# Optimization experiments

Measured on AMD Instinct MI355X. Metric: run time of the kernel, lower is better.

The kernel has to match this reference:

```python
import jax, jax.numpy as jnp
import numpy as np

B = 64          # batch
C = 80          # num_classes
IN_CH = 300     # word-embedding channel
J = 8192        # JOINT_EMB_SIZE (linear_intermediate)
S = 8           # pooling_stride
OUT = J // S    # out_in_tmp = 1024


def setup_inputs() -> dict:
    key = jax.random.key(0)
    ks = jax.random.split(key, 8)
    w = lambda k, sh: jax.random.normal(k, sh, jnp.float32) * 0.02
    return {
        "feature": jax.random.normal(ks[0], (B, 2048, 14, 14), jnp.float32),
        "inp": jax.random.normal(ks[1], (1, C, IN_CH), jnp.float32),
        "A": jax.random.uniform(ks[2], (C, C), jnp.float32),  # positive co-occurrence adjacency
        "W_gc1": w(ks[3], (IN_CH, 1024)),
        "W_gc2": w(ks[4], (1024, 2048)),
        "W_img": w(ks[5], (J, 2048)),
        "b_img": jnp.zeros((J,), jnp.float32),
        "W_cls": w(ks[6], (J, 2048)),
        "b_cls": jnp.zeros((J,), jnp.float32),
        "W_ml": w(ks[7], (C, C * OUT)),
        "b_ml": jnp.zeros((C,), jnp.float32),
    }


def reference(feature, inp, A, W_gc1, W_gc2, W_img, b_img, W_cls, b_cls, W_ml, b_ml):
    # backbone output -> MaxPool2d(14,14) over a 14x14 map == global spatial max
    feat = feature.max(axis=(2, 3))                       # [B, 2048]

    # gen_adj(A).detach(): D = diag(rowsum(A)^-0.5); adj = D @ A.T @ D
    dinv = jnp.sum(A, axis=1) ** -0.5                     # [C]
    adj = jax.lax.stop_gradient(A.T * dinv[:, None] * dinv[None, :])  # [C, C]

    # two GCN layers on label embeddings
    x = adj @ (inp[0] @ W_gc1)                            # [C, 1024]
    x = jax.nn.leaky_relu(x, 0.2)
    x = adj @ (x @ W_gc2)                                 # [C, 2048]

    # MFB bilinear fusion (vectorized form of the nested batch/class loops;
    # dropout is identity in eval mode)
    img = feat @ W_img.T + b_img                          # [B, J]
    cls = x @ W_cls.T + b_cls                             # [C, J]
    # sum-pool over the stride axis of the elementwise product:
    # iq[b,c,o] = sum_s img[b,o*S+s] * cls[c,o*S+s]
    pooled = jnp.einsum('bos,cos->bco',
                        img.reshape(B, OUT, S),
                        cls.reshape(C, OUT, S))           # [B, C, OUT]
    # torch.cat order over class columns -> c-major flatten, then ML_fc_layer
    out = pooled.reshape(B, C * OUT) @ W_ml.T + b_ml      # [B, C]
    return out
```

## Files before the change

### kernel.cpp

```cpp
#include <hip/hip_runtime.h>
#include <hip/hip_bf16.h>
#include <cstdint>
#include <cstddef>

typedef float  f32x4  __attribute__((ext_vector_type(4)));
typedef __bf16 bf16x8 __attribute__((ext_vector_type(8)));
typedef unsigned short u16x8 __attribute__((ext_vector_type(8)));

__device__ __forceinline__ unsigned short f2bf(float f) {
    unsigned u = __float_as_uint(f);
    u += 0x7FFFu + ((u >> 16) & 1u);
    return (unsigned short)(u >> 16);
}


constexpr size_t OFF_FEATB = 0;
constexpr size_t OFF_X2B   = 262144;
constexpr size_t OFF_XB    = 425984;
constexpr size_t OFF_IMG   = 753664;
constexpr size_t OFF_CLS   = 2850816;
constexpr size_t OFF_G     = 5472256;


__device__ __forceinline__ void maxpool_role(int vbid, const float* __restrict__ feature,
                                             unsigned short* __restrict__ featb) {
    int wave = threadIdx.x >> 6, lane = threadIdx.x & 63;
    int r = lane >> 4, q = lane & 15;
    int rbase = vbid * 64 + wave * 4 + r;
    const float4* p[4];
    #pragma unroll
    for (int it = 0; it < 4; ++it)
        p[it] = (const float4*)(feature + (size_t)(rbase + it * 16) * 196);
    float4 v[4][4];
    #pragma unroll
    for (int it = 0; it < 4; ++it) {
        v[it][0] = p[it][q];
        v[it][1] = p[it][q + 16];
        v[it][2] = p[it][q + 32];
        v[it][3] = p[it][48];
    }
    #pragma unroll
    for (int it = 0; it < 4; ++it) {
        float4 a = v[it][0], b = v[it][1], c = v[it][2], d = v[it][3];
        float m = fmaxf(fmaxf(fmaxf(fmaxf(a.x, a.y), fmaxf(a.z, a.w)),
                              fmaxf(fmaxf(b.x, b.y), fmaxf(b.z, b.w))),
                        fmaxf(fmaxf(fmaxf(c.x, c.y), fmaxf(c.z, c.w)),
                              fmaxf(fmaxf(d.x, d.y), fmaxf(d.z, d.w))));
        #pragma unroll
        for (int off = 1; off < 16; off <<= 1) m = fmaxf(m, __shfl_xor(m, off));
        if (q == 0) featb[rbase + it * 16] = f2bf(m);
    }
}

__device__ __forceinline__ void gcn_front_role(int idx, const float* __restrict__ inp,
                                               const float* __restrict__ W1,
                                               const float* __restrict__ A,
                                               unsigned short* __restrict__ x2b,
                                               float* smem) {
    float* adjs = smem;
    float* y0s  = smem + 6400;
    float* x1s  = smem + 7040;
    float* dinv = smem + 7680;
    int t = threadIdx.x;
    int j = t & 7, slot = t >> 3;
    int j0 = idx * 8;
    int c0 = slot, c1 = slot + 32, c2 = slot + 64;
    bool has3 = (slot < 16);

    if (t < 80) {
        const float4* ar = (const float4*)(A + t * 80);
        float4 s4 = {0.f, 0.f, 0.f, 0.f};
        #pragma unroll
        for (int q = 0; q < 20; q++) {
            float4 v = ar[q];
            s4.x += v.x; s4.y += v.y; s4.z += v.z; s4.w += v.w;
        }
        dinv[t] = 1.0f / sqrtf(s4.x + s4.y + s4.z + s4.w);
    }
    __syncthreads();
    for (int i = t; i < 6400; i += 256) {
        int r = i / 80, cc = i % 80;
        adjs[i] = A[cc * 80 + r] * dinv[r] * dinv[cc];
    }

    const float* wcol = W1 + j0 + j;
    const float* i0 = inp + c0 * 300;
    const float* i1 = inp + c1 * 300;
    const float* i2 = inp + c2 * 300;
    float a0 = 0.f, a1 = 0.f, a2 = 0.f;
    for (int k = 0; k < 300; k += 4) {
        float w[4], p0[4], p1[4], p2[4];
        #pragma unroll
        for (int u = 0; u < 4; u++) w[u] = wcol[(size_t)(k + u) * 1024];
        #pragma unroll
        for (int u = 0; u < 4; u++) p0[u] = i0[k + u];
        #pragma unroll
        for (int u = 0; u < 4; u++) p1[u] = i1[k + u];
        if (has3) {
            #pragma unroll
            for (int u = 0; u < 4; u++) p2[u] = i2[k + u];
        }
        #pragma unroll
        for (int u = 0; u < 4; u++) {
            a0 = fmaf(p0[u], w[u], a0);
            a1 = fmaf(p1[u], w[u], a1);
            if (has3) a2 = fmaf(p2[u], w[u], a2);
        }
    }
    __syncthreads();
    y0s[c0 * 8 + j] = a0;
    y0s[c1 * 8 + j] = a1;
    if (has3) y0s[c2 * 8 + j] = a2;
    __syncthreads();

    float b0 = 0.f, b1 = 0.f, b2 = 0.f;
    #pragma unroll 4
    for (int e = 0; e < 80; e++) {
        float y = y0s[e * 8 + j];
        b0 = fmaf(adjs[c0 * 80 + e], y, b0);
        b1 = fmaf(adjs[c1 * 80 + e], y, b1);
        if (has3) b2 = fmaf(adjs[c2 * 80 + e], y, b2);
    }
    if (b0 < 0.f) b0 *= 0.2f;
    if (b1 < 0.f) b1 *= 0.2f;
    if (b2 < 0.f) b2 *= 0.2f;
    x1s[c0 * 8 + j] = b0;
    x1s[c1 * 8 + j] = b1;
    if (has3) x1s[c2 * 8 + j] = b2;
    __syncthreads();

    float d0 = 0.f, d1 = 0.f, d2 = 0.f;
    #pragma unroll 4
    for (int e = 0; e < 80; e++) {
        float x = x1s[e * 8 + j];
        d0 = fmaf(adjs[c0 * 80 + e], x, d0);
        d1 = fmaf(adjs[c1 * 80 + e], x, d1);
        if (has3) d2 = fmaf(adjs[c2 * 80 + e], x, d2);
    }
    x2b[c0 * 1024 + j0 + j] = f2bf(d0);
    x2b[c1 * 1024 + j0 + j] = f2bf(d1);
    if (has3) x2b[c2 * 1024 + j0 + j] = f2bf(d2);
}

template <int MF>
__device__ __forceinline__ void gemm_block(int bx, const unsigned short* __restrict__ X,
                                           const float* __restrict__ W,
                                           const float* __restrict__ bias,
                                           float* __restrict__ outf,
                                           unsigned short* __restrict__ outb,
                                           int N, int K, float (*red)[64][21]) {
    int tid = threadIdx.x;
    int ks = tid >> 6, lane = tid & 63;
    int n = bx * 16 + (lane & 15);
    int rowa = lane & 15;
    int koff = (lane >> 4) * 8;
    int Kc = K >> 2;
    int k0 = ks * Kc;

    f32x4 acc[MF];
    #pragma unroll
    for (int i = 0; i < MF; i++) acc[i] = (f32x4)(0.f);

    const float* wrow = W + (size_t)n * K;

    #pragma unroll 2
    for (int k = k0; k < k0 + Kc; k += 32) {
        float4 w0 = *(const float4*)(wrow + k + koff);
        float4 w1 = *(const float4*)(wrow + k + koff + 4);
        u16x8 bu;
        bu[0] = f2bf(w0.x); bu[1] = f2bf(w0.y); bu[2] = f2bf(w0.z); bu[3] = f2bf(w0.w);
        bu[4] = f2bf(w1.x); bu[5] = f2bf(w1.y); bu[6] = f2bf(w1.z); bu[7] = f2bf(w1.w);
        bf16x8 bf = __builtin_bit_cast(bf16x8, bu);
        #pragma unroll
        for (int mf = 0; mf < MF; mf++) {
            u16x8 au = *(const u16x8*)(X + (size_t)(mf * 16 + rowa) * K + k + koff);
            acc[mf] = __builtin_amdgcn_mfma_f32_16x16x32_bf16(
                __builtin_bit_cast(bf16x8, au), bf, acc[mf], 0, 0, 0);
        }
    }

    #pragma unroll
    for (int mf = 0; mf < MF; mf++)
        #pragma unroll
        for (int i = 0; i < 4; i++)
            red[ks][lane][mf * 4 + i] = acc[mf][i];
    __syncthreads();

    int lane2 = tid & 63, sg = tid >> 6;
    int n2 = bx * 16 + (lane2 & 15);
    float b = bias ? bias[n2] : 0.f;
    #pragma unroll
    for (int mf = 0; mf < MF; mf++) {
        int slot = mf * 4 + sg;
        float s = red[0][lane2][slot] + red[1][lane2][slot]
                + red[2][lane2][slot] + red[3][lane2][slot] + b;
        int row = mf * 16 + (lane2 >> 4) * 4 + sg;
        size_t o = (size_t)row * N + n2;
        if (outf) outf[o] = s;
        if (outb) outb[o] = f2bf(s);
    }
}

template <int MF>
__device__ __forceinline__ void gemm_block_kn(int bx, const unsigned short* __restrict__ X,
                                              const float* __restrict__ Wkn,
                                              const float* __restrict__ bias,
                                              float* __restrict__ outf,
                                              unsigned short* __restrict__ outb,
                                              int N, int K, float (*red)[64][21]) {
    int tid = threadIdx.x;
    int ks = tid >> 6, lane = tid & 63;
    int n = bx * 16 + (lane & 15);
    int rowa = lane & 15;
    int koff = (lane >> 4) * 8;
    int Kc = K >> 2;
    int k0 = ks * Kc;

    f32x4 acc[MF];
    #pragma unroll
    for (int i = 0; i < MF; i++) acc[i] = (f32x4)(0.f);

    #pragma unroll 2
    for (int k = k0; k < k0 + Kc; k += 32) {
        float w[8];
        #pragma unroll
        for (int i = 0; i < 8; i++) w[i] = Wkn[(size_t)(k + koff + i) * N + n];
        u16x8 bu;
        #pragma unroll
        for (int i = 0; i < 8; i++) bu[i] = f2bf(w[i]);
        bf16x8 bf = __builtin_bit_cast(bf16x8, bu);
        #pragma unroll
        for (int mf = 0; mf < MF; mf++) {
            u16x8 au = *(const u16x8*)(X + (size_t)(mf * 16 + rowa) * K + k + koff);
            acc[mf] = __builtin_amdgcn_mfma_f32_16x16x32_bf16(
                __builtin_bit_cast(bf16x8, au), bf, acc[mf], 0, 0, 0);
        }
    }

    #pragma unroll
    for (int mf = 0; mf < MF; mf++)
        #pragma unroll
        for (int i = 0; i < 4; i++)
            red[ks][lane][mf * 4 + i] = acc[mf][i];
    __syncthreads();

    int lane2 = tid & 63, sg = tid >> 6;
    int n2 = bx * 16 + (lane2 & 15);
    float b = bias ? bias[n2] : 0.f;
    #pragma unroll
    for (int mf = 0; mf < MF; mf++) {
        int slot = mf * 4 + sg;
        float s = red[0][lane2][slot] + red[1][lane2][slot]
                + red[2][lane2][slot] + red[3][lane2][slot] + b;
        int row = mf * 16 + (lane2 >> 4) * 4 + sg;
        size_t o = (size_t)row * N + n2;
        if (outf) outf[o] = s;
        if (outb) outb[o] = f2bf(s);
    }
}


__global__ __launch_bounds__(256, 2) void kD1(const float* __restrict__ feature,
                                              unsigned short* __restrict__ featb,
                                              const float* __restrict__ inp,
                                              const float* __restrict__ W1,
                                              const float* __restrict__ A,
                                              unsigned short* __restrict__ x2b) {
    __shared__ __align__(16) float smem[7760];
    int b = blockIdx.x;
    if (b < 128) gcn_front_role(b, inp, W1, A, x2b, smem);
    else         maxpool_role(b - 128, feature, featb);
}

__global__ __launch_bounds__(256, 4) void kD2(const unsigned short* __restrict__ featb,
                                              const float* __restrict__ W_img,
                                              const float* __restrict__ b_img,
                                              float* __restrict__ img,
                                              const unsigned short* __restrict__ x2b,
                                              const float* __restrict__ W_gc2,
                                              unsigned short* __restrict__ xb) {
    __shared__ __align__(16) float red[4][64][21];
    int b = blockIdx.x;
    if (b < 512) gemm_block<4>(b, featb, W_img, b_img, img, nullptr, 8192, 2048, red);
    else         gemm_block_kn<5>(b - 512, x2b, W_gc2, nullptr, nullptr, xb, 2048, 1024, red);
}

__global__ __launch_bounds__(256, 4) void kD3(const unsigned short* __restrict__ xb,
                                              const float* __restrict__ W_cls,
                                              const float* __restrict__ b_cls,
                                              float* __restrict__ cls) {
    __shared__ __align__(16) float red[4][64][21];
    gemm_block<5>(blockIdx.x, xb, W_cls, b_cls, cls, nullptr, 8192, 2048, red);
}

__global__ __launch_bounds__(256, 4) void kD4(const float* __restrict__ cls,
                                              const float* __restrict__ W_ml,
                                              float* __restrict__ G) {
    __shared__ __align__(16) float smem[8 * 80 * 16];
    float (*wml)[80][16] = (float (*)[80][16])smem;
    int idx = blockIdx.x;
    int o0  = (idx & 63) * 16;
    int c2b = (idx >> 6) * 8;
    int j0  = o0 * 8;
    for (int i = threadIdx.x; i < 8 * 80 * 16; i += 256) {
        int ol = i & 15, c = (i >> 4) % 80, c2 = i / 1280;
        wml[c2][c][ol] = W_ml[(size_t)(c2b + c2) * 81920 + c * 1024 + o0 + ol];
    }
    __syncthreads();
    int jl  = threadIdx.x & 127;
    int c2h = (threadIdx.x >> 7) * 4;
    int ol  = jl >> 3;
    float acc[4] = {0.f, 0.f, 0.f, 0.f};
    for (int c = 0; c < 80; c++) {
        float cv = cls[(size_t)c * 8192 + j0 + jl];
        #pragma unroll
        for (int i = 0; i < 4; i++) acc[i] = fmaf(cv, wml[c2h + i][c][ol], acc[i]);
    }
    #pragma unroll
    for (int i = 0; i < 4; i++) G[(size_t)(c2b + c2h + i) * 8192 + j0 + jl] = acc[i];
}

__global__ __launch_bounds__(256, 2) void kD5(const float* __restrict__ img,
                                              const float* __restrict__ G,
                                              const float* __restrict__ b_ml,
                                              float* __restrict__ out) {
    __shared__ float sm[4][8];
    int b = blockIdx.x / 10, cg = blockIdx.x % 10;
    int kc = threadIdx.x >> 6, lane = threadIdx.x & 63;
    const float* ib = img + (size_t)b * 8192 + kc * 2048;
    const float* gb = G + (size_t)(cg * 8) * 8192 + kc * 2048;
    float acc[8] = {0.f, 0.f, 0.f, 0.f, 0.f, 0.f, 0.f, 0.f};
    #pragma unroll
    for (int step = 0; step < 8; step++) {
        int k = step * 256 + lane * 4;
        float4 iv = *(const float4*)(ib + k);
        float4 gv[8];
        #pragma unroll
        for (int i = 0; i < 8; i++) gv[i] = *(const float4*)(gb + (size_t)i * 8192 + k);
        #pragma unroll
        for (int i = 0; i < 8; i++) {
            acc[i] = fmaf(iv.x, gv[i].x, acc[i]);
            acc[i] = fmaf(iv.y, gv[i].y, acc[i]);
            acc[i] = fmaf(iv.z, gv[i].z, acc[i]);
            acc[i] = fmaf(iv.w, gv[i].w, acc[i]);
        }
    }
    #pragma unroll
    for (int i = 0; i < 8; i++) {
        float v = acc[i];
        #pragma unroll
        for (int off = 32; off; off >>= 1) v += __shfl_xor(v, off);
        if (lane == 0) sm[kc][i] = v;
    }
    __syncthreads();
    if (threadIdx.x < 8) {
        int i = threadIdx.x;
        float s = b_ml[cg * 8 + i] + sm[0][i] + sm[1][i] + sm[2][i] + sm[3][i];
        out[(size_t)b * 80 + cg * 8 + i] = s;
    }
}

extern "C" void kernel_launch(void* const* d_in, const int* in_sizes, int n_in,
                              void* d_out, int out_size, void* d_ws, size_t ws_size,
                              hipStream_t stream) {
    (void)in_sizes; (void)n_in; (void)out_size; (void)ws_size;
    const float* feature = (const float*)d_in[0];
    const float* inp     = (const float*)d_in[1];
    const float* A       = (const float*)d_in[2];
    const float* W_gc1   = (const float*)d_in[3];
    const float* W_gc2   = (const float*)d_in[4];
    const float* W_img   = (const float*)d_in[5];
    const float* b_img   = (const float*)d_in[6];
    const float* W_cls   = (const float*)d_in[7];
    const float* b_cls   = (const float*)d_in[8];
    const float* W_ml    = (const float*)d_in[9];
    const float* b_ml    = (const float*)d_in[10];
    float* out = (float*)d_out;
    char*  ws  = (char*)d_ws;

    unsigned short* featb = (unsigned short*)(ws + OFF_FEATB);
    unsigned short* x2b   = (unsigned short*)(ws + OFF_X2B);
    unsigned short* xb    = (unsigned short*)(ws + OFF_XB);
    float* img  = (float*)(ws + OFF_IMG);
    float* cls  = (float*)(ws + OFF_CLS);
    float* G    = (float*)(ws + OFF_G);

    kD1<<<2176, 256, 0, stream>>>(feature, featb, inp, W_gc1, A, x2b);
    kD2<<<640,  256, 0, stream>>>(featb, W_img, b_img, img, x2b, W_gc2, xb);
    kD3<<<512,  256, 0, stream>>>(xb, W_cls, b_cls, cls);
    kD4<<<640,  256, 0, stream>>>(cls, W_ml, G);
    kD5<<<640,  256, 0, stream>>>(img, G, b_ml, out);
}
```

Baseline: 149.8 us.

## Fold adjacency normalization into scaling and shrink maxpool blocks for occupancy

```diff
diff --git a/kernel.cpp b/kernel.cpp
--- a/kernel.cpp
+++ b/kernel.cpp
@@ -25,31 +25,27 @@
 __device__ __forceinline__ void maxpool_role(int vbid, const float* __restrict__ feature,
                                              unsigned short* __restrict__ featb) {
     int wave = threadIdx.x >> 6, lane = threadIdx.x & 63;
-    int r = lane >> 4, q = lane & 15;
-    int rbase = vbid * 64 + wave * 4 + r;
-    const float4* p[4];
-    #pragma unroll
-    for (int it = 0; it < 4; ++it)
-        p[it] = (const float4*)(feature + (size_t)(rbase + it * 16) * 196);
-    float4 v[4][4];
-    #pragma unroll
-    for (int it = 0; it < 4; ++it) {
-        v[it][0] = p[it][q];
-        v[it][1] = p[it][q + 16];
-        v[it][2] = p[it][q + 32];
-        v[it][3] = p[it][48];
-    }
-    #pragma unroll
-    for (int it = 0; it < 4; ++it) {
-        float4 a = v[it][0], b = v[it][1], c = v[it][2], d = v[it][3];
-        float m = fmaxf(fmaxf(fmaxf(fmaxf(a.x, a.y), fmaxf(a.z, a.w)),
-                              fmaxf(fmaxf(b.x, b.y), fmaxf(b.z, b.w))),
-                        fmaxf(fmaxf(fmaxf(c.x, c.y), fmaxf(c.z, c.w)),
-                              fmaxf(fmaxf(d.x, d.y), fmaxf(d.z, d.w))));
-        #pragma unroll
-        for (int off = 1; off < 16; off <<= 1) m = fmaxf(m, __shfl_xor(m, off));
-        if (q == 0) featb[rbase + it * 16] = f2bf(m);
-    }
+    int r = lane >> 3, q = lane & 7;
+    int row = vbid * 32 + wave * 8 + r;
+    const float4* p = (const float4*)(feature + (size_t)row * 196);
+    float4 v0 = p[q];
+    float4 v1 = p[q + 8];
+    float4 v2 = p[q + 16];
+    float4 v3 = p[q + 24];
+    float4 v4 = p[q + 32];
+    float4 v5 = p[q + 40];
+    float4 v6 = p[48];
+    float m0 = fmaxf(fmaxf(v0.x, v0.y), fmaxf(v0.z, v0.w));
+    float m1 = fmaxf(fmaxf(v1.x, v1.y), fmaxf(v1.z, v1.w));
+    float m2 = fmaxf(fmaxf(v2.x, v2.y), fmaxf(v2.z, v2.w));
+    float m3 = fmaxf(fmaxf(v3.x, v3.y), fmaxf(v3.z, v3.w));
+    float m4 = fmaxf(fmaxf(v4.x, v4.y), fmaxf(v4.z, v4.w));
+    float m5 = fmaxf(fmaxf(v5.x, v5.y), fmaxf(v5.z, v5.w));
+    float m6 = fmaxf(fmaxf(v6.x, v6.y), fmaxf(v6.z, v6.w));
+    float m = fmaxf(fmaxf(fmaxf(m0, m1), fmaxf(m2, m3)), fmaxf(fmaxf(m4, m5), m6));
+    #pragma unroll
+    for (int off = 1; off < 8; off <<= 1) m = fmaxf(m, __shfl_xor(m, off));
+    if (q == 0) featb[row] = f2bf(m);
 }
 
 __device__ __forceinline__ void gcn_front_role(int idx, const float* __restrict__ inp,
@@ -57,10 +53,9 @@
                                                const float* __restrict__ A,
                                                unsigned short* __restrict__ x2b,
                                                float* smem) {
-    float* adjs = smem;
-    float* y0s  = smem + 6400;
-    float* x1s  = smem + 7040;
-    float* dinv = smem + 7680;
+    float* dinv = smem;
+    float* ys   = smem + 80;
+    float* xs   = smem + 720;
     int t = threadIdx.x;
     int j = t & 7, slot = t >> 3;
     int j0 = idx * 8;
@@ -76,11 +71,6 @@
             s4.x += v.x; s4.y += v.y; s4.z += v.z; s4.w += v.w;
         }
         dinv[t] = 1.0f / sqrtf(s4.x + s4.y + s4.z + s4.w);
-    }
-    __syncthreads();
-    for (int i = t; i < 6400; i += 256) {
-        int r = i / 80, cc = i % 80;
-        adjs[i] = A[cc * 80 + r] * dinv[r] * dinv[cc];
     }
 
     const float* wcol = W1 + j0 + j;
@@ -108,38 +98,42 @@
         }
     }
     __syncthreads();
-    y0s[c0 * 8 + j] = a0;
-    y0s[c1 * 8 + j] = a1;
-    if (has3) y0s[c2 * 8 + j] = a2;
+    ys[c0 * 8 + j] = dinv[c0] * a0;
+    ys[c1 * 8 + j] = dinv[c1] * a1;
+    if (has3) ys[c2 * 8 + j] = dinv[c2] * a2;
     __syncthreads();
 
     float b0 = 0.f, b1 = 0.f, b2 = 0.f;
     #pragma unroll 4
     for (int e = 0; e < 80; e++) {
-        float y = y0s[e * 8 + j];
-        b0 = fmaf(adjs[c0 * 80 + e], y, b0);
-        b1 = fmaf(adjs[c1 * 80 + e], y, b1);
-        if (has3) b2 = fmaf(adjs[c2 * 80 + e], y, b2);
-    }
+        float y = ys[e * 8 + j];
+        b0 = fmaf(A[e * 80 + c0], y, b0);
+        b1 = fmaf(A[e * 80 + c1], y, b1);
+        if (has3) b2 = fmaf(A[e * 80 + c2], y, b2);
+    }
+    b0 *= dinv[c0];
+    b1 *= dinv[c1];
+    b2 *= has3 ? dinv[c2] : 0.f;
     if (b0 < 0.f) b0 *= 0.2f;
     if (b1 < 0.f) b1 *= 0.2f;
     if (b2 < 0.f) b2 *= 0.2f;
-    x1s[c0 * 8 + j] = b0;
-    x1s[c1 * 8 + j] = b1;
-    if (has3) x1s[c2 * 8 + j] = b2;
+    __syncthreads();
+    xs[c0 * 8 + j] = dinv[c0] * b0;
+    xs[c1 * 8 + j] = dinv[c1] * b1;
+    if (has3) xs[c2 * 8 + j] = dinv[c2] * b2;
     __syncthreads();
 
     float d0 = 0.f, d1 = 0.f, d2 = 0.f;
     #pragma unroll 4
     for (int e = 0; e < 80; e++) {
-        float x = x1s[e * 8 + j];
-        d0 = fmaf(adjs[c0 * 80 + e], x, d0);
-        d1 = fmaf(adjs[c1 * 80 + e], x, d1);
-        if (has3) d2 = fmaf(adjs[c2 * 80 + e], x, d2);
-    }
-    x2b[c0 * 1024 + j0 + j] = f2bf(d0);
-    x2b[c1 * 1024 + j0 + j] = f2bf(d1);
-    if (has3) x2b[c2 * 1024 + j0 + j] = f2bf(d2);
+        float x = xs[e * 8 + j];
+        d0 = fmaf(A[e * 80 + c0], x, d0);
+        d1 = fmaf(A[e * 80 + c1], x, d1);
+        if (has3) d2 = fmaf(A[e * 80 + c2], x, d2);
+    }
+    x2b[c0 * 1024 + j0 + j] = f2bf(d0 * dinv[c0]);
+    x2b[c1 * 1024 + j0 + j] = f2bf(d1 * dinv[c1]);
+    if (has3) x2b[c2 * 1024 + j0 + j] = f2bf(d2 * dinv[c2]);
 }
 
 template <int MF>
@@ -260,13 +254,13 @@
 }
 
 
-__global__ __launch_bounds__(256, 2) void kD1(const float* __restrict__ feature,
+__global__ __launch_bounds__(256, 4) void kD1(const float* __restrict__ feature,
                                               unsigned short* __restrict__ featb,
                                               const float* __restrict__ inp,
                                               const float* __restrict__ W1,
                                               const float* __restrict__ A,
                                               unsigned short* __restrict__ x2b) {
-    __shared__ __align__(16) float smem[7760];
+    __shared__ __align__(16) float smem[1360];
     int b = blockIdx.x;
     if (b < 128) gcn_front_role(b, inp, W1, A, x2b, smem);
     else         maxpool_role(b - 128, feature, featb);
@@ -385,7 +379,7 @@
     float* cls  = (float*)(ws + OFF_CLS);
     float* G    = (float*)(ws + OFF_G);
 
-    kD1<<<2176, 256, 0, stream>>>(feature, featb, inp, W_gc1, A, x2b);
+    kD1<<<4224, 256, 0, stream>>>(feature, featb, inp, W_gc1, A, x2b);
     kD2<<<640,  256, 0, stream>>>(featb, W_img, b_img, img, x2b, W_gc2, xb);
     kD3<<<512,  256, 0, stream>>>(xb, W_cls, b_cls, cls);
     kD4<<<640,  256, 0, stream>>>(cls, W_ml, G);
```

Measured after the change: 157.1 us (median of 2 runs). 4.8% more time.
